# Performance work log

Measured on AMD Instinct MI355X. Metric: run time of the kernel, lower is better.

## Reference

```python
import jax, jax.numpy as jnp
import numpy as np

N, F_DIM, H, MAX_STEPS = 768, 256, 128, 100


def normalize_adj(adj):
    # add self loops, symmetric normalization D^{-1/2} (A+I) D^{-1/2}
    a = adj + jnp.eye(adj.shape[0], dtype=adj.dtype)
    d = a.sum(axis=-1)
    d_inv_sqrt = jnp.where(d > 0, jax.lax.rsqrt(d), 0.0)
    return d_inv_sqrt[:, None] * a * d_inv_sqrt[None, :]


def gcn_layer(h, a_norm, weight):
    return jax.nn.relu(a_norm @ h @ weight)


def setup_inputs() -> dict:
    key = jax.random.key(0)
    ks = jax.random.split(key, 8)
    xavier = lambda k, shp: jax.random.uniform(k, shp, jnp.float32,
                                               -np.sqrt(6.0 / (shp[0] + shp[1])),
                                               np.sqrt(6.0 / (shp[0] + shp[1])))
    return {
        "x": jax.random.normal(ks[0], (N, F_DIM), jnp.float32),
        "adj_noisy": jax.random.uniform(ks[1], (N, N), jnp.float32),
        "w1": xavier(ks[2], (F_DIM, H)),
        "w2": xavier(ks[3], (H, H)),
        "time_emb": jax.random.normal(ks[4], (MAX_STEPS, H), jnp.float32),
        "we1": xavier(ks[5], (3 * H, H)),
        "be1": jnp.zeros((H,), jnp.float32),
        "we2": xavier(ks[6], (H, 1)),
        "be2": jnp.zeros((1,), jnp.float32),
        "t": 50,
    }


def reference(x, adj_noisy, w1, w2, time_emb, we1, be1, we2, be2, t):
    a_norm = normalize_adj(adj_noisy)
    h = gcn_layer(x, a_norm, w1)            # (N, H)
    h = gcn_layer(h, a_norm, w2)            # (N, H)
    t_emb = time_emb[t]                     # (H,)
    # edge_mlp layer 1 on concat([h_i, h_j, t_emb]) decomposed to avoid (N,N,3H):
    # concat @ we1 == h_i @ we1[:H] + h_j @ we1[H:2H] + t_emb @ we1[2H:]
    p = h @ we1[:H]                         # (N, H) contribution from h_i
    q = h @ we1[H:2 * H]                    # (N, H) contribution from h_j
    c = t_emb @ we1[2 * H:] + be1           # (H,)  contribution from t_emb + bias
    z = jax.nn.relu(p[:, None, :] + q[None, :, :] + c)   # (N, N, H)
    logits = (z @ we2)[..., 0] + be2[0]     # (N, N)
    adj_pred = jax.nn.sigmoid(logits)
    return (adj_pred + adj_pred.T) / 2
```

## Files before the change

kernel.cpp:

```cpp
#include <hip/hip_runtime.h>

#define NN 768
#define FD 256
#define HD 128

__device__ __forceinline__ float relu(float x) { return x > 0.f ? x : 0.f; }
__device__ __forceinline__ void fma4(float4& a, float s, float4 v) {
    a.x = fmaf(s, v.x, a.x); a.y = fmaf(s, v.y, a.y);
    a.z = fmaf(s, v.z, a.z); a.w = fmaf(s, v.w, a.w);
}
__device__ __forceinline__ float rdot(float4 a, float4 b, float4 w) {
    float s = relu(a.x + b.x) * w.x;
    s = fmaf(relu(a.y + b.y), w.y, s);
    s = fmaf(relu(a.z + b.z), w.z, s);
    s = fmaf(relu(a.w + b.w), w.w, s);
    return s;
}

__global__ __launch_bounds__(768) void k_prep(
        const float* __restrict__ x, const float* __restrict__ adj,
        const float* __restrict__ w1, const float* __restrict__ temb,
        const float* __restrict__ we1, const float* __restrict__ be1,
        const int* __restrict__ tptr, float* __restrict__ dinv,
        float* __restrict__ cvec, float* __restrict__ t1D) {
    int b = blockIdx.x, tid = threadIdx.x;
    if (b == 256) {
        __shared__ float ts[HD];
        if (tid < HD) ts[tid] = temb[tptr[0] * HD + tid];
        __syncthreads();
        if (tid < HD) {
            float a0 = be1[tid], a1 = 0.f, a2 = 0.f, a3 = 0.f;
            for (int m = 0; m < HD; m += 4) {
                a0 = fmaf(ts[m + 0], we1[(2 * HD + m + 0) * HD + tid], a0);
                a1 = fmaf(ts[m + 1], we1[(2 * HD + m + 1) * HD + tid], a1);
                a2 = fmaf(ts[m + 2], we1[(2 * HD + m + 2) * HD + tid], a2);
                a3 = fmaf(ts[m + 3], we1[(2 * HD + m + 3) * HD + tid], a3);
            }
            cvec[tid] = (a0 + a1) + (a2 + a3);
        }
        return;
    }
    int i0 = b * 3;
    __shared__ float xs[3][FD];
    __shared__ float part[3][2][HD];
    __shared__ float red[12];
    __shared__ float sdi[3];
    if (tid < 192) {
        int row = tid >> 6, m4 = tid & 63;
        *(float4*)&xs[row][m4 * 4] = *(const float4*)&x[(i0 + row) * FD + m4 * 4];
    }
    {
        int r2 = tid >> 8, s = tid & 255;
        float sum = 0.f;
        if (s < 192) {
            float4 a = *(const float4*)&adj[(i0 + r2) * NN + s * 4];
            sum = (a.x + a.y) + (a.z + a.w);
        }
#pragma unroll
        for (int off = 32; off > 0; off >>= 1) sum += __shfl_down(sum, off, 64);
        if ((tid & 63) == 0) red[tid >> 6] = sum;
    }
    __syncthreads();
    if (tid < 3) {
        float t = (red[4 * tid] + red[4 * tid + 1]) + (red[4 * tid + 2] + red[4 * tid + 3]);
        float d = rsqrtf(t + 1.f);
        sdi[tid] = d; dinv[i0 + tid] = d;
    }
    __syncthreads();
    int r = tid >> 8, half = (tid >> 7) & 1, k = tid & 127;
    float a0 = 0.f, a1 = 0.f, a2 = 0.f, a3 = 0.f;
    for (int g = 128 * half; g < 128 * half + 128; g += 16) {
        float wv[16];
#pragma unroll
        for (int u = 0; u < 16; ++u) wv[u] = w1[(g + u) * HD + k];
#pragma unroll
        for (int u = 0; u < 16; ++u) {
            float xv = xs[r][g + u];
            if ((u & 3) == 0) a0 = fmaf(xv, wv[u], a0);
            else if ((u & 3) == 1) a1 = fmaf(xv, wv[u], a1);
            else if ((u & 3) == 2) a2 = fmaf(xv, wv[u], a2);
            else a3 = fmaf(xv, wv[u], a3);
        }
    }
    part[r][half][k] = (a0 + a1) + (a2 + a3);
    __syncthreads();
    if (half == 0) t1D[(i0 + r) * HD + k] = sdi[r] * (part[r][0][k] + part[r][1][k]);
}

__device__ __forceinline__ void gcn_agg(
        float* __restrict__ a0s, float* __restrict__ a1s, float* __restrict__ a2s,
        float (*part)[3][HD], float (*gs)[HD],
        const float* __restrict__ adj, const float* __restrict__ tin,
        const float* __restrict__ dinv, int i0, int tid) {
    for (int j = tid; j < NN; j += 256) {
        a0s[j] = adj[(i0 + 0) * NN + j];
        a1s[j] = adj[(i0 + 1) * NN + j];
        a2s[j] = adj[(i0 + 2) * NN + j];
    }
    __syncthreads();
    int k4 = tid & 31, jc = tid >> 5;
    float4 acc0 = {0,0,0,0}, acc1 = {0,0,0,0}, acc2 = {0,0,0,0};
    const float* tb = tin + k4 * 4;
#pragma unroll 4
    for (int jj = 0; jj < 96; ++jj) {
        int j = jc * 96 + jj;
        float4 tv = *(const float4*)&tb[j * HD];
        fma4(acc0, a0s[j], tv);
        fma4(acc1, a1s[j], tv);
        fma4(acc2, a2s[j], tv);
    }
    *(float4*)&part[jc][0][k4 * 4] = acc0;
    *(float4*)&part[jc][1][k4 * 4] = acc1;
    *(float4*)&part[jc][2][k4 * 4] = acc2;
    __syncthreads();
    for (int idx = tid; idx < 3 * HD; idx += 256) {
        int r = idx >> 7, k = idx & 127;
        float s = tin[(i0 + r) * HD + k];
#pragma unroll
        for (int c = 0; c < 8; ++c) s += part[c][r][k];
        gs[r][k] = relu(dinv[i0 + r] * s);
    }
    __syncthreads();
}

__global__ __launch_bounds__(256) void k_layer1(
        const float* __restrict__ adj, const float* __restrict__ t1,
        const float* __restrict__ dinv, const float* __restrict__ w2,
        float* __restrict__ t2) {
    __shared__ float a0s[NN], a1s[NN], a2s[NN];
    __shared__ float part[8][3][HD];
    __shared__ float gs[3][HD];
    int tid = threadIdx.x, i0 = blockIdx.x * 3;
    gcn_agg(a0s, a1s, a2s, part, gs, adj, t1, dinv, i0, tid);
    for (int idx = tid; idx < 3 * HD; idx += 256) {
        int r = idx >> 7, k = idx & 127;
        float acc = 0.f;
        const float* wc = w2 + k;
#pragma unroll
        for (int m4 = 0; m4 < 32; ++m4) {
            float4 gv = *(float4*)&gs[r][m4 * 4];
            acc = fmaf(gv.x, wc[(m4 * 4 + 0) * HD], acc);
            acc = fmaf(gv.y, wc[(m4 * 4 + 1) * HD], acc);
            acc = fmaf(gv.z, wc[(m4 * 4 + 2) * HD], acc);
            acc = fmaf(gv.w, wc[(m4 * 4 + 3) * HD], acc);
        }
        t2[(i0 + r) * HD + k] = dinv[i0 + r] * acc;
    }
}

__global__ __launch_bounds__(256) void k_layer2(
        const float* __restrict__ adj, const float* __restrict__ t2,
        const float* __restrict__ dinv, const float* __restrict__ we1,
        const float* __restrict__ cvec, float* __restrict__ p, float* __restrict__ q) {
    __shared__ float a0s[NN], a1s[NN], a2s[NN];
    __shared__ float part[8][3][HD];
    __shared__ float gs[3][HD];
    int tid = threadIdx.x, i0 = blockIdx.x * 3;
    gcn_agg(a0s, a1s, a2s, part, gs, adj, t2, dinv, i0, tid);
    for (int idx = tid; idx < 3 * HD; idx += 256) {
        int r = idx >> 7, k = idx & 127;
        float ap = 0.f, aq = 0.f;
        const float* wp = we1 + k;
        const float* wq = we1 + HD * HD + k;
#pragma unroll
        for (int m4 = 0; m4 < 32; ++m4) {
            float4 gv = *(float4*)&gs[r][m4 * 4];
            ap = fmaf(gv.x, wp[(m4 * 4 + 0) * HD], ap); aq = fmaf(gv.x, wq[(m4 * 4 + 0) * HD], aq);
            ap = fmaf(gv.y, wp[(m4 * 4 + 1) * HD], ap); aq = fmaf(gv.y, wq[(m4 * 4 + 1) * HD], aq);
            ap = fmaf(gv.z, wp[(m4 * 4 + 2) * HD], ap); aq = fmaf(gv.z, wq[(m4 * 4 + 2) * HD], aq);
            ap = fmaf(gv.w, wp[(m4 * 4 + 3) * HD], ap); aq = fmaf(gv.w, wq[(m4 * 4 + 3) * HD], aq);
        }
        p[(i0 + r) * HD + k] = ap + cvec[k];
        q[(i0 + r) * HD + k] = aq;
    }
}

__global__ __launch_bounds__(256) void k_pair(
        const float* __restrict__ p, const float* __restrict__ q,
        const float* __restrict__ we2, const float* __restrict__ be2,
        float* __restrict__ out) {
    int t = blockIdx.x;
    int bj = (int)((sqrtf(8.f * t + 1.f) - 1.f) * 0.5f);
    while ((bj + 1) * (bj + 2) / 2 <= t) ++bj;
    while (bj * (bj + 1) / 2 > t) --bj;
    int bi = t - bj * (bj + 1) / 2;
    int i0 = bi * 32, j0 = bj * 32;
    __shared__ float spi[32][68], sqi[32][68], spj[32][68], sqj[32][68];
    __shared__ float w2s[HD];
    int tid = threadIdx.x;
    int tx = tid & 15, ty = tid >> 4;
    if (tid < HD) w2s[tid] = we2[tid];
    float accij[2][2] = {{0.f, 0.f}, {0.f, 0.f}};
    float accji[2][2] = {{0.f, 0.f}, {0.f, 0.f}};
    for (int h = 0; h < 2; ++h) {
        __syncthreads();
        int kb = h * 64;
        for (int idx = tid; idx < 512; idx += 256) {
            int r = idx >> 4, c4 = idx & 15;
            *(float4*)&spi[r][c4 * 4] = *(const float4*)&p[(i0 + r) * HD + kb + c4 * 4];
            *(float4*)&sqi[r][c4 * 4] = *(const float4*)&q[(i0 + r) * HD + kb + c4 * 4];
            *(float4*)&spj[r][c4 * 4] = *(const float4*)&p[(j0 + r) * HD + kb + c4 * 4];
            *(float4*)&sqj[r][c4 * 4] = *(const float4*)&q[(j0 + r) * HD + kb + c4 * 4];
        }
        __syncthreads();
#pragma unroll 8
        for (int k4 = 0; k4 < 16; ++k4) {
            float4 w = *(float4*)&w2s[kb + k4 * 4];
            float4 Pi0 = *(float4*)&spi[2 * ty + 0][k4 * 4];
            float4 Pi1 = *(float4*)&spi[2 * ty + 1][k4 * 4];
            float4 Qi0 = *(float4*)&sqi[2 * ty + 0][k4 * 4];
            float4 Qi1 = *(float4*)&sqi[2 * ty + 1][k4 * 4];
            float4 Pj0 = *(float4*)&spj[2 * tx + 0][k4 * 4];
            float4 Pj1 = *(float4*)&spj[2 * tx + 1][k4 * 4];
            float4 Qj0 = *(float4*)&sqj[2 * tx + 0][k4 * 4];
            float4 Qj1 = *(float4*)&sqj[2 * tx + 1][k4 * 4];
            accij[0][0] += rdot(Pi0, Qj0, w); accji[0][0] += rdot(Pj0, Qi0, w);
            accij[0][1] += rdot(Pi0, Qj1, w); accji[0][1] += rdot(Pj1, Qi0, w);
            accij[1][0] += rdot(Pi1, Qj0, w); accji[1][0] += rdot(Pj0, Qi1, w);
            accij[1][1] += rdot(Pi1, Qj1, w); accji[1][1] += rdot(Pj1, Qi1, w);
        }
    }
    float bias = be2[0];
#pragma unroll
    for (int e = 0; e < 2; ++e)
#pragma unroll
        for (int f = 0; f < 2; ++f) {
            int i = i0 + 2 * ty + e, j = j0 + 2 * tx + f;
            float lij = accij[e][f] + bias, lji = accji[e][f] + bias;
            float v = 0.5f * (1.f / (1.f + __expf(-lij)) + 1.f / (1.f + __expf(-lji)));
            out[i * NN + j] = v;
            out[j * NN + i] = v;
        }
}

extern "C" void kernel_launch(void* const* d_in, const int* in_sizes, int n_in,
                              void* d_out, int out_size, void* d_ws, size_t ws_size,
                              hipStream_t stream) {
    const float* x    = (const float*)d_in[0];
    const float* adj  = (const float*)d_in[1];
    const float* w1   = (const float*)d_in[2];
    const float* w2   = (const float*)d_in[3];
    const float* temb = (const float*)d_in[4];
    const float* we1  = (const float*)d_in[5];
    const float* be1  = (const float*)d_in[6];
    const float* we2  = (const float*)d_in[7];
    const float* be2  = (const float*)d_in[8];
    const int* tptr   = (const int*)d_in[9];
    float* out        = (float*)d_out;

    float* ws   = (float*)d_ws;
    float* dinv = ws;
    float* cvec = ws + 768;
    float* t1   = ws + 1024;
    float* t2   = t1 + NN * HD;
    float* p    = t2 + NN * HD;
    float* q    = p + NN * HD;

    k_prep  <<<257, 768, 0, stream>>>(x, adj, w1, temb, we1, be1, tptr, dinv, cvec, t1);
    k_layer1<<<256, 256, 0, stream>>>(adj, t1, dinv, w2, t2);
    k_layer2<<<256, 256, 0, stream>>>(adj, t2, dinv, we1, cvec, p, q);
    k_pair  <<<300, 256, 0, stream>>>(p, q, we2, be2, out);
}
```

Before: 126.4 us.

## Widen GCN aggregation blocks and retile pair kernel into smaller coalesced tiles

The two GCN layer kernels move to 512 threads per block, splitting the neighbour reduction across 16 partial chunks instead of 8, so each thread walks fewer rows and latency is hidden better. The pair kernel drops from 32x32 tiles with 2x2 outputs per thread to 16x16 tiles with one output per thread. That raises the grid from 300 to 1176 blocks, which should balance better across the CUs, and it loads the full 128-wide feature rows in one shot instead of two halves. The mirrored output is now written through a shared-memory transpose so both stores are coalesced. The cost is less register reuse per shared-memory load in the pair kernel, and more reduction traffic in the layer kernels.

```diff
diff --git a/kernel.cpp b/kernel.cpp
--- a/kernel.cpp
+++ b/kernel.cpp
@@ -87,12 +87,12 @@
     if (half == 0) t1D[(i0 + r) * HD + k] = sdi[r] * (part[r][0][k] + part[r][1][k]);
 }
 
-__device__ __forceinline__ void gcn_agg(
+__device__ __forceinline__ void gcn_agg512(
         float* __restrict__ a0s, float* __restrict__ a1s, float* __restrict__ a2s,
         float (*part)[3][HD], float (*gs)[HD],
         const float* __restrict__ adj, const float* __restrict__ tin,
         const float* __restrict__ dinv, int i0, int tid) {
-    for (int j = tid; j < NN; j += 256) {
+    for (int j = tid; j < NN; j += 512) {
         a0s[j] = adj[(i0 + 0) * NN + j];
         a1s[j] = adj[(i0 + 1) * NN + j];
         a2s[j] = adj[(i0 + 2) * NN + j];
@@ -102,8 +102,8 @@
     float4 acc0 = {0,0,0,0}, acc1 = {0,0,0,0}, acc2 = {0,0,0,0};
     const float* tb = tin + k4 * 4;
 #pragma unroll 4
-    for (int jj = 0; jj < 96; ++jj) {
-        int j = jc * 96 + jj;
+    for (int jj = 0; jj < 48; ++jj) {
+        int j = jc * 48 + jj;
         float4 tv = *(const float4*)&tb[j * HD];
         fma4(acc0, a0s[j], tv);
         fma4(acc1, a1s[j], tv);
@@ -113,27 +113,27 @@
     *(float4*)&part[jc][1][k4 * 4] = acc1;
     *(float4*)&part[jc][2][k4 * 4] = acc2;
     __syncthreads();
-    for (int idx = tid; idx < 3 * HD; idx += 256) {
-        int r = idx >> 7, k = idx & 127;
+    if (tid < 3 * HD) {
+        int r = tid >> 7, k = tid & 127;
         float s = tin[(i0 + r) * HD + k];
 #pragma unroll
-        for (int c = 0; c < 8; ++c) s += part[c][r][k];
+        for (int c = 0; c < 16; ++c) s += part[c][r][k];
         gs[r][k] = relu(dinv[i0 + r] * s);
     }
     __syncthreads();
 }
 
-__global__ __launch_bounds__(256) void k_layer1(
+__global__ __launch_bounds__(512) void k_layer1(
         const float* __restrict__ adj, const float* __restrict__ t1,
         const float* __restrict__ dinv, const float* __restrict__ w2,
         float* __restrict__ t2) {
     __shared__ float a0s[NN], a1s[NN], a2s[NN];
-    __shared__ float part[8][3][HD];
+    __shared__ float part[16][3][HD];
     __shared__ float gs[3][HD];
     int tid = threadIdx.x, i0 = blockIdx.x * 3;
-    gcn_agg(a0s, a1s, a2s, part, gs, adj, t1, dinv, i0, tid);
-    for (int idx = tid; idx < 3 * HD; idx += 256) {
-        int r = idx >> 7, k = idx & 127;
+    gcn_agg512(a0s, a1s, a2s, part, gs, adj, t1, dinv, i0, tid);
+    if (tid < 3 * HD) {
+        int r = tid >> 7, k = tid & 127;
         float acc = 0.f;
         const float* wc = w2 + k;
 #pragma unroll
@@ -148,17 +148,17 @@
     }
 }
 
-__global__ __launch_bounds__(256) void k_layer2(
+__global__ __launch_bounds__(512) void k_layer2(
         const float* __restrict__ adj, const float* __restrict__ t2,
         const float* __restrict__ dinv, const float* __restrict__ we1,
         const float* __restrict__ cvec, float* __restrict__ p, float* __restrict__ q) {
     __shared__ float a0s[NN], a1s[NN], a2s[NN];
-    __shared__ float part[8][3][HD];
+    __shared__ float part[16][3][HD];
     __shared__ float gs[3][HD];
     int tid = threadIdx.x, i0 = blockIdx.x * 3;
-    gcn_agg(a0s, a1s, a2s, part, gs, adj, t2, dinv, i0, tid);
-    for (int idx = tid; idx < 3 * HD; idx += 256) {
-        int r = idx >> 7, k = idx & 127;
+    gcn_agg512(a0s, a1s, a2s, part, gs, adj, t2, dinv, i0, tid);
+    if (tid < 3 * HD) {
+        int r = tid >> 7, k = tid & 127;
         float ap = 0.f, aq = 0.f;
         const float* wp = we1 + k;
         const float* wq = we1 + HD * HD + k;
@@ -184,53 +184,39 @@
     while ((bj + 1) * (bj + 2) / 2 <= t) ++bj;
     while (bj * (bj + 1) / 2 > t) --bj;
     int bi = t - bj * (bj + 1) / 2;
-    int i0 = bi * 32, j0 = bj * 32;
-    __shared__ float spi[32][68], sqi[32][68], spj[32][68], sqj[32][68];
+    int i0 = bi * 16, j0 = bj * 16;
+    __shared__ float spi[16][132], sqi[16][132], spj[16][132], sqj[16][132];
     __shared__ float w2s[HD];
+    __shared__ float vt[16][17];
     int tid = threadIdx.x;
+    if (tid < HD) w2s[tid] = we2[tid];
+    for (int idx = tid; idx < 512; idx += 256) {
+        int r = idx >> 5, c4 = idx & 31;
+        *(float4*)&spi[r][c4 * 4] = *(const float4*)&p[(i0 + r) * HD + c4 * 4];
+        *(float4*)&sqi[r][c4 * 4] = *(const float4*)&q[(i0 + r) * HD + c4 * 4];
+        *(float4*)&spj[r][c4 * 4] = *(const float4*)&p[(j0 + r) * HD + c4 * 4];
+        *(float4*)&sqj[r][c4 * 4] = *(const float4*)&q[(j0 + r) * HD + c4 * 4];
+    }
+    __syncthreads();
     int tx = tid & 15, ty = tid >> 4;
-    if (tid < HD) w2s[tid] = we2[tid];
-    float accij[2][2] = {{0.f, 0.f}, {0.f, 0.f}};
-    float accji[2][2] = {{0.f, 0.f}, {0.f, 0.f}};
-    for (int h = 0; h < 2; ++h) {
-        __syncthreads();
-        int kb = h * 64;
-        for (int idx = tid; idx < 512; idx += 256) {
-            int r = idx >> 4, c4 = idx & 15;
-            *(float4*)&spi[r][c4 * 4] = *(const float4*)&p[(i0 + r) * HD + kb + c4 * 4];
-            *(float4*)&sqi[r][c4 * 4] = *(const float4*)&q[(i0 + r) * HD + kb + c4 * 4];
-            *(float4*)&spj[r][c4 * 4] = *(const float4*)&p[(j0 + r) * HD + kb + c4 * 4];
-            *(float4*)&sqj[r][c4 * 4] = *(const float4*)&q[(j0 + r) * HD + kb + c4 * 4];
-        }
-        __syncthreads();
+    float aij = 0.f, aji = 0.f;
 #pragma unroll 8
-        for (int k4 = 0; k4 < 16; ++k4) {
-            float4 w = *(float4*)&w2s[kb + k4 * 4];
-            float4 Pi0 = *(float4*)&spi[2 * ty + 0][k4 * 4];
-            float4 Pi1 = *(float4*)&spi[2 * ty + 1][k4 * 4];
-            float4 Qi0 = *(float4*)&sqi[2 * ty + 0][k4 * 4];
-            float4 Qi1 = *(float4*)&sqi[2 * ty + 1][k4 * 4];
-            float4 Pj0 = *(float4*)&spj[2 * tx + 0][k4 * 4];
-            float4 Pj1 = *(float4*)&spj[2 * tx + 1][k4 * 4];
-            float4 Qj0 = *(float4*)&sqj[2 * tx + 0][k4 * 4];
-            float4 Qj1 = *(float4*)&sqj[2 * tx + 1][k4 * 4];
-            accij[0][0] += rdot(Pi0, Qj0, w); accji[0][0] += rdot(Pj0, Qi0, w);
-            accij[0][1] += rdot(Pi0, Qj1, w); accji[0][1] += rdot(Pj1, Qi0, w);
-            accij[1][0] += rdot(Pi1, Qj0, w); accji[1][0] += rdot(Pj0, Qi1, w);
-            accij[1][1] += rdot(Pi1, Qj1, w); accji[1][1] += rdot(Pj1, Qi1, w);
-        }
+    for (int k4 = 0; k4 < 32; ++k4) {
+        float4 w  = *(float4*)&w2s[k4 * 4];
+        float4 Pi = *(float4*)&spi[ty][k4 * 4];
+        float4 Qj = *(float4*)&sqj[tx][k4 * 4];
+        float4 Pj = *(float4*)&spj[tx][k4 * 4];
+        float4 Qi = *(float4*)&sqi[ty][k4 * 4];
+        aij += rdot(Pi, Qj, w);
+        aji += rdot(Pj, Qi, w);
     }
     float bias = be2[0];
-#pragma unroll
-    for (int e = 0; e < 2; ++e)
-#pragma unroll
-        for (int f = 0; f < 2; ++f) {
-            int i = i0 + 2 * ty + e, j = j0 + 2 * tx + f;
-            float lij = accij[e][f] + bias, lji = accji[e][f] + bias;
-            float v = 0.5f * (1.f / (1.f + __expf(-lij)) + 1.f / (1.f + __expf(-lji)));
-            out[i * NN + j] = v;
-            out[j * NN + i] = v;
-        }
+    float v = 0.5f * (1.f / (1.f + __expf(-(aij + bias)))
+                    + 1.f / (1.f + __expf(-(aji + bias))));
+    out[(i0 + ty) * NN + (j0 + tx)] = v;
+    vt[tx][ty] = v;
+    __syncthreads();
+    out[(j0 + ty) * NN + (i0 + tx)] = vt[ty][tx];
 }
 
 extern "C" void kernel_launch(void* const* d_in, const int* in_sizes, int n_in,
@@ -257,7 +243,7 @@
     float* q    = p + NN * HD;
 
     k_prep  <<<257, 768, 0, stream>>>(x, adj, w1, temb, we1, be1, tptr, dinv, cvec, t1);
-    k_layer1<<<256, 256, 0, stream>>>(adj, t1, dinv, w2, t2);
-    k_layer2<<<256, 256, 0, stream>>>(adj, t2, dinv, we1, cvec, p, q);
-    k_pair  <<<300, 256, 0, stream>>>(p, q, we2, be2, out);
-}
+    k_layer1<<<256, 512, 0, stream>>>(adj, t1, dinv, w2, t2);
+    k_layer2<<<256, 512, 0, stream>>>(adj, t2, dinv, we1, cvec, p, q);
+    k_pair  <<<1176, 256, 0, stream>>>(p, q, we2, be2, out);
+}
```

Result: slower. 163.4 us (+29.2%).
